# Kernel optimization log

Hardware: AMD Instinct MI355X
Metric: run time of the kernel (lower is better)

The kernel has to match this reference:

```python
import jax, jax.numpy as jnp
import numpy as np

N = 20000   # nodes per type per hop
E = 200000  # edges per relation per hop
H = 512     # node_feature_hid_len
FU = 512    # raw user feature len
FI = 256    # raw item feature len
NUM_RES = 2
NUM_DNN = 2


def setup_inputs() -> dict:
    key = jax.random.key(0)
    ks = iter(jax.random.split(key, 64))
    p = lambda shape: jax.random.normal(next(ks), shape, dtype=jnp.float32) * 0.05
    inp = {}
    # features per hop per type
    for h in range(3):
        inp[f'feat_user_h{h}'] = jax.random.normal(next(ks), (N, FU), dtype=jnp.float32)
        inp[f'feat_item_h{h}'] = jax.random.normal(next(ks), (N, FI), dtype=jnp.float32)
    del inp['feat_user_h2_']; 


def _unused():
    pass

# rebuild setup_inputs cleanly (above stub replaced)

def setup_inputs() -> dict:
    key = jax.random.key(0)
    ks = iter(jax.random.split(key, 64))
    p = lambda shape: jax.random.normal(next(ks), shape, dtype=jnp.float32) * 0.05
    inp = {}
    for h in range(3):
        inp[f'feat_user_h{h}'] = jax.random.normal(next(ks), (N, FU), dtype=jnp.float32)
        inp[f'feat_item_h{h}'] = jax.random.normal(next(ks), (N, FI), dtype=jnp.float32)
    for name in ('edges_UI_h0', 'edges_IU_h0', 'edges_UI_h1', 'edges_IU_h1'):
        inp[name] = jax.random.randint(next(ks), (2, E), 0, N, dtype=jnp.int32)
    # per-node-type input transforms
    inp['W_user'] = p((FU, H)); inp['b_user'] = jnp.zeros((H,), jnp.float32)
    inp['W_item'] = p((FI, H)); inp['b_item'] = jnp.zeros((H,), jnp.float32)
    # per-relation GATConv params, stacked over 2 relations [UI, IU]
    inp['gat_feat_W'] = p((2, H, H)); inp['gat_feat_b'] = jnp.zeros((2, H), jnp.float32)
    inp['gat_att_w'] = p((2, 2 * H)); inp['gat_att_b'] = jnp.zeros((2,), jnp.float32)
    inp['gat_bias'] = jnp.zeros((2, H), jnp.float32)
    # Res_DNN params
    inp['prep_W'] = p((H, H)); inp['prep_b'] = jnp.zeros((H,), jnp.float32)
    inp['dnn_W'] = p((NUM_RES, NUM_DNN, H, H)); inp['dnn_b'] = jnp.zeros((NUM_RES, NUM_DNN, H), jnp.float32)
    inp['dnn_ln_g'] = jnp.ones((NUM_RES, NUM_DNN, H), jnp.float32); inp['dnn_ln_b'] = jnp.zeros((NUM_RES, NUM_DNN, H), jnp.float32)
    inp['res_ln_g'] = jnp.ones((NUM_RES, H), jnp.float32); inp['res_ln_b'] = jnp.zeros((NUM_RES, H), jnp.float32)
    inp['cls_W'] = p((H, 1)); inp['cls_b'] = jnp.zeros((1,), jnp.float32)
    return inp


def _ln(x, g, b, eps=1e-5):
    mu = jnp.mean(x, axis=-1, keepdims=True)
    var = jnp.mean((x - mu) ** 2, axis=-1, keepdims=True)
    return (x - mu) * jax.lax.rsqrt(var + eps) * g + b


def _gat(head_h, tail_h, edges, fW, fb, aw, ab, bias):
    # GATConv: feat_linear on both sides, tanh edge attention, per-source-row
    # sparse softmax, scatter-weighted sum of transformed tail features.
    s = head_h @ fW + fb            # [Nh, H]
    t = tail_h @ fW + fb            # [Nt, H]
    src, tgt = edges[0], edges[1]
    # att(cat([s_e, t_e])) split into per-node scores (same math as concat @ aw)
    e = jnp.tanh((s @ aw[:H])[src] + (t @ aw[H:])[tgt] + ab)  # [E]
    nh = head_h.shape[0]
    m = jax.ops.segment_max(e, src, num_segments=nh)
    ex = jnp.exp(e - m[src])
    den = jax.ops.segment_sum(ex, src, num_segments=nh)
    alpha = ex / den[src]
    hp = jax.ops.segment_sum(alpha[:, None] * t[tgt], src, num_segments=nh)
    return hp + bias


def _forward(feat_user_h0, feat_item_h0, feat_user_h1, feat_item_h1,
             feat_user_h2, feat_item_h2,
             W_user, b_user, W_item, b_item,
             gat_feat_W, gat_feat_b, gat_att_w, gat_att_b, gat_bias,
             prep_W, prep_b, dnn_W, dnn_b, dnn_ln_g, dnn_ln_b,
             res_ln_g, res_ln_b, cls_W, cls_b,
             edges_UI_h0, edges_IU_h0, edges_UI_h1, edges_IU_h1):
    def gat(r, head, tail, edges):
        return _gat(head, tail, edges, gat_feat_W[r], gat_feat_b[r],
                    gat_att_w[r], gat_att_b[r], gat_bias[r])
    # hop 2 (deepest): transformed source features
    su = feat_user_h2 @ W_user + b_user
    si = feat_item_h2 @ W_item + b_item
    # hop 1
    hu = feat_user_h1 @ W_user + b_user
    hi = feat_item_h1 @ W_item + b_item
    su_new = (hu + gat(0, hu, si, edges_UI_h1)) * 0.5  # mean of [self, UI agg]
    si_new = (hi + gat(1, hi, su, edges_IU_h1)) * 0.5
    su, si = su_new, si_new
    # hop 0
    hu = feat_user_h0 @ W_user + b_user
    hi = feat_item_h0 @ W_item + b_item
    su_new = (hu + gat(0, hu, si, edges_UI_h0)) * 0.5
    su = su_new  # target node type = 'user' (first key)
    # Res_DNN head
    x = su @ prep_W + prep_b
    for r in range(NUM_RES):
        sc = x
        for d in range(NUM_DNN):
            x = _ln(jnp.tanh(x @ dnn_W[r, d] + dnn_b[r, d]), dnn_ln_g[r, d], dnn_ln_b[r, d])
        x = _ln(jnp.tanh(sc + x), res_ln_g[r], res_ln_b[r])
    return jax.nn.sigmoid(x @ cls_W + cls_b)  # [N, 1]


def reference(feat_user_h0, feat_item_h0, feat_user_h1, feat_item_h1,
              feat_user_h2, feat_item_h2,
              edges_UI_h0, edges_IU_h0, edges_UI_h1, edges_IU_h1,
              W_user, b_user, W_item, b_item,
              gat_feat_W, gat_feat_b, gat_att_w, gat_att_b, gat_bias,
              prep_W, prep_b, dnn_W, dnn_b, dnn_ln_g, dnn_ln_b,
              res_ln_g, res_ln_b, cls_W, cls_b):
    return _forward(feat_user_h0, feat_item_h0, feat_user_h1, feat_item_h1,
                    feat_user_h2, feat_item_h2,
                    W_user, b_user, W_item, b_item,
                    gat_feat_W, gat_feat_b, gat_att_w, gat_att_b, gat_bias,
                    prep_W, prep_b, dnn_W, dnn_b, dnn_ln_g, dnn_ln_b,
                    res_ln_g, res_ln_b, cls_W, cls_b,
                    edges_UI_h0, edges_IU_h0, edges_UI_h1, edges_IU_h1)
```

## Files before the change

kernel.cpp:

```cpp
#include <hip/hip_runtime.h>
#include <math.h>

#define NN 20000
#define NE 200000
#define HH 512

typedef __attribute__((ext_vector_type(8))) short short8v;
typedef __attribute__((ext_vector_type(4))) float f32x4;

__device__ inline short f2bf(float f) {
    union { float f; unsigned u; } v; v.f = f;
    unsigned r = (v.u + 0x7fffu + ((v.u >> 16) & 1u)) >> 16;
    return (short)r;
}
__device__ inline float bf2f(short s) {
    union { unsigned u; float f; } v;
    v.u = ((unsigned)(unsigned short)s) << 16;
    return v.f;
}

__device__ inline void gload_lds16(const void* g, void* l) {
    __builtin_amdgcn_global_load_lds(
        (const __attribute__((address_space(1))) void*)g,
        (__attribute__((address_space(3))) void*)l, 16, 0, 0);
}

__global__ __launch_bounds__(256)
void f2b_all(const float* __restrict__ fu2, const float* __restrict__ fu0,
             const float* __restrict__ fi1, short* __restrict__ S0,
             short* __restrict__ XI1, int nh8)
{
    int i = blockIdx.x * 256 + threadIdx.x;
    const float* src; short* dst; int off;
    if (i < nh8)            { src = fu2; dst = S0;                    off = i; }
    else if (i < 2 * nh8)   { src = fu0; dst = S0 + (size_t)nh8 * 8;  off = i - nh8; }
    else if (i < 2 * nh8 + nh8 / 2) { src = fi1; dst = XI1;           off = i - 2 * nh8; }
    else return;
    const float4* p = (const float4*)src + (size_t)off * 2;
    float4 a = p[0], b = p[1];
    short8v s;
    s[0] = f2bf(a.x); s[1] = f2bf(a.y); s[2] = f2bf(a.z); s[3] = f2bf(a.w);
    s[4] = f2bf(b.x); s[5] = f2bf(b.y); s[6] = f2bf(b.z); s[7] = f2bf(b.w);
    ((short8v*)dst)[off] = s;
}

__global__ __launch_bounds__(256)
void wtr_all(const float* __restrict__ Wu, const float* __restrict__ Wi,
             const float* __restrict__ gfW, const float* __restrict__ prW,
             const float* __restrict__ dW,
             short* __restrict__ WTu, short* __restrict__ WTi,
             short* __restrict__ WTg0, short* __restrict__ WTg1,
             short* __restrict__ WTpr, short* __restrict__ WTd)
{
    __shared__ float t[32][33];
    int z = blockIdx.z;
    const float* src; short* dst; int K;
    if (z == 0)      { src = Wu;  dst = WTu;  K = 512; }
    else if (z == 1) { src = Wi;  dst = WTi;  K = 256; }
    else if (z == 2) { src = gfW; dst = WTg0; K = 512; }
    else if (z == 3) { src = gfW + (size_t)512 * 512; dst = WTg1; K = 512; }
    else if (z == 4) { src = prW; dst = WTpr; K = 512; }
    else { src = dW + (size_t)(z - 5) * 512 * 512;
           dst = WTd + (size_t)(z - 5) * 512 * 512; K = 512; }
    int by = blockIdx.y * 32;
    if (by >= K) return;
    int bx = blockIdx.x * 32;
    int tx = threadIdx.x, ty = threadIdx.y;
    for (int i = ty; i < 32; i += 8)
        t[i][tx] = src[(size_t)(by + i) * 512 + bx + tx];
    __syncthreads();
    for (int i = ty; i < 32; i += 8)
        dst[(size_t)(bx + i) * K + by + tx] = f2bf(t[tx][i]);
}

__global__ __launch_bounds__(256)
void mfma_lin(const short* __restrict__ X, const short* __restrict__ WT,
              const float* __restrict__ bias, float* __restrict__ outF,
              short* __restrict__ outB, int M, int K,
              const short* __restrict__ rdH, const short* __restrict__ rdT,
              const float* __restrict__ rduv, const float* __restrict__ rds0,
              float* __restrict__ rdss, float* __restrict__ rdts, int rdN)
{
    __shared__ short8v pool[4096];

    const int tid = threadIdx.x;
    const int lane = tid & 63;
    const int w = tid >> 6;

    const int nby = (M + 127) >> 7;
    const int nwg = nby << 2;
    int id = blockIdx.x;

    if (id >= nwg) {
        int row = (id - nwg) * 4 + w;
        if (row >= rdN) return;
        short8v h = ((const short8v*)(rdH + (size_t)row * HH))[lane];
        short8v t = ((const short8v*)(rdT + (size_t)row * HH))[lane];
        const float4* up = (const float4*)rduv + lane * 2;
        const float4* vp = (const float4*)(rduv + HH) + lane * 2;
        float4 u0 = up[0], u1 = up[1], v0 = vp[0], v1 = vp[1];
        float a = bf2f(h[0])*u0.x + bf2f(h[1])*u0.y + bf2f(h[2])*u0.z + bf2f(h[3])*u0.w
                + bf2f(h[4])*u1.x + bf2f(h[5])*u1.y + bf2f(h[6])*u1.z + bf2f(h[7])*u1.w;
        float b = bf2f(t[0])*v0.x + bf2f(t[1])*v0.y + bf2f(t[2])*v0.z + bf2f(t[3])*v0.w
                + bf2f(t[4])*v1.x + bf2f(t[5])*v1.y + bf2f(t[6])*v1.z + bf2f(t[7])*v1.w;
#pragma unroll
        for (int m = 32; m >= 1; m >>= 1) {
            a += __shfl_xor(a, m);
            b += __shfl_xor(b, m);
        }
        if (lane == 0) { rdss[row] = a + rds0[0]; rdts[row] = b + rds0[1]; }
        return;
    }

    const int q = nwg >> 3, r = nwg & 7;
    int xcd = id & 7, wi = id >> 3;
    int wgid = (xcd < r ? xcd * (q + 1) : r * (q + 1) + (xcd - r) * q) + wi;
    const int col0 = (wgid & 3) * 128;
    const int row0 = (wgid >> 2) * 128;

    const int wr = (w >> 1) * 64;
    const int wc = (w & 1) * 64;

    const short* gsrc[8];
#pragma unroll
    for (int g = 0; g < 8; ++g) {
        int p = w * 512 + g * 64 + lane;
        if (p < 1024) {
            int row = p >> 3;
            int c = (p & 7) ^ (row & 7);
            int ga = row0 + row; if (ga >= M) ga = M - 1;
            gsrc[g] = X + (size_t)ga * K + c * 8;
        } else {
            int qq = p - 1024;
            int col = qq >> 3;
            int c = (qq & 7) ^ (col & 7);
            gsrc[g] = WT + (size_t)(col0 + col) * K + c * 8;
        }
    }

    int ar[2][4], br[2][4];
#pragma unroll
    for (int kk = 0; kk < 2; ++kk) {
#pragma unroll
        for (int i = 0; i < 4; ++i) {
            int rr = wr + i * 16 + (lane & 15);
            ar[kk][i] = rr * 8 + ((kk * 4 + (lane >> 4)) ^ (rr & 7));
            int nn = wc + i * 16 + (lane & 15);
            br[kk][i] = 1024 + nn * 8 + ((kk * 4 + (lane >> 4)) ^ (nn & 7));
        }
    }

    f32x4 acc[4][4];
#pragma unroll
    for (int i = 0; i < 4; ++i)
#pragma unroll
        for (int j = 0; j < 4; ++j)
            acc[i][j] = (f32x4){0.f, 0.f, 0.f, 0.f};

    auto stage = [&](int buf, int kk) {
        short8v* base = pool + buf * 2048 + w * 512;
#pragma unroll
        for (int g = 0; g < 8; ++g)
            gload_lds16(gsrc[g] + kk, base + g * 64);
    };

    const int nt = K >> 6;
    stage(0, 0);
    if (nt > 1) stage(1, 64);
    int cur = 0;
    for (int t = 0; t < nt; ++t) {
        if (t + 1 < nt) asm volatile("s_waitcnt vmcnt(8)" ::: "memory");
        else            asm volatile("s_waitcnt vmcnt(0)" ::: "memory");
        __builtin_amdgcn_s_barrier();
        const short8v* S = pool + cur * 2048;
#pragma unroll
        for (int kk = 0; kk < 2; ++kk) {
            short8v af[4], bf[4];
#pragma unroll
            for (int i = 0; i < 4; ++i) af[i] = S[ar[kk][i]];
#pragma unroll
            for (int j = 0; j < 4; ++j) bf[j] = S[br[kk][j]];
#pragma unroll
            for (int i = 0; i < 4; ++i)
#pragma unroll
                for (int j = 0; j < 4; ++j)
                    acc[i][j] = __builtin_amdgcn_mfma_f32_16x16x32_bf16(af[i], bf[j], acc[i][j], 0, 0, 0);
        }
        __builtin_amdgcn_s_barrier();
        if (t + 2 < nt) stage(cur, (t + 2) * 64);
        cur ^= 1;
    }

    float bj[4];
#pragma unroll
    for (int j = 0; j < 4; ++j)
        bj[j] = bias[col0 + wc + j * 16 + (lane & 15)];

    if (outF) {
#pragma unroll
        for (int i = 0; i < 4; ++i) {
#pragma unroll
            for (int rr = 0; rr < 4; ++rr) {
                int row = row0 + wr + i * 16 + (lane >> 4) * 4 + rr;
                if (row < M) {
                    float* op = outF + (size_t)row * HH + col0 + wc + (lane & 15);
#pragma unroll
                    for (int j = 0; j < 4; ++j) op[j * 16] = acc[i][j][rr] + bj[j];
                }
            }
        }
    }
    if (outB) {
        short* lt = (short*)pool;
#pragma unroll
        for (int i = 0; i < 4; ++i)
#pragma unroll
            for (int rr = 0; rr < 4; ++rr) {
                int lrow = wr + i * 16 + (lane >> 4) * 4 + rr;
#pragma unroll
                for (int j = 0; j < 4; ++j)
                    lt[lrow * 128 + wc + j * 16 + (lane & 15)] = f2bf(acc[i][j][rr] + bj[j]);
            }
        __syncthreads();
#pragma unroll
        for (int k = 0; k < 8; ++k) {
            int row = (tid >> 4) + 16 * k;
            int seg = tid & 15;
            int grow = row0 + row;
            if (grow < M) {
                short8v vv = *(short8v*)(lt + row * 128 + seg * 8);
                *(short8v*)(outB + (size_t)grow * HH + col0 + seg * 8) = vv;
            }
        }
    }
}

__global__ __launch_bounds__(256)
void gat_pre2(const float* __restrict__ gfW, const float* __restrict__ gfb,
              const float* __restrict__ gaw, float* __restrict__ uvall,
              float* __restrict__ s0t0all)
{
    int rrel = blockIdx.y;
    const float* fW = gfW + (size_t)rrel * HH * HH;
    const float* fb = gfb + rrel * HH;
    const float* aw = gaw + (size_t)rrel * 2 * HH;
    float* uv = uvall + rrel * 1024;
    float* s0t0 = s0t0all + rrel * 4;
    int row = blockIdx.x * 4 + (threadIdx.x >> 6);
    int lane = threadIdx.x & 63;
    const float4* ah = (const float4*)aw;
    const float4* at = (const float4*)(aw + HH);
    const float4* fp;
    if (row < 512)       fp = (const float4*)(fW + (size_t)row * HH);
    else if (row == 512) fp = (const float4*)fb;
    else return;
    float du = 0.f, dv = 0.f;
#pragma unroll
    for (int l = 0; l < 2; ++l) {
        int idx = lane * 2 + l;
        float4 f = fp[idx], a = ah[idx], b = at[idx];
        du += f.x*a.x + f.y*a.y + f.z*a.z + f.w*a.w;
        dv += f.x*b.x + f.y*b.y + f.z*b.z + f.w*b.w;
    }
#pragma unroll
    for (int m = 32; m >= 1; m >>= 1) {
        du += __shfl_xor(du, m);
        dv += __shfl_xor(dv, m);
    }
    if (lane == 0) {
        if (row < 512) { uv[row] = du; uv[512 + row] = dv; }
        else           { s0t0[0] = du; s0t0[1] = dv; }
    }
}

__global__ __launch_bounds__(256)
void count2_kernel(const int* __restrict__ s0, const int* __restrict__ s1,
                   int* __restrict__ c0, int* __restrict__ c1, int E)
{
    int i = blockIdx.x * blockDim.x + threadIdx.x;
    if (i < E) atomicAdd(&c0[s0[i]], 1);
    else if (i < 2 * E) atomicAdd(&c1[s1[i - E]], 1);
}

__global__ __launch_bounds__(1024)
void scan2_kernel(const int* __restrict__ c0, const int* __restrict__ c1,
                  int* __restrict__ o0, int* __restrict__ o1,
                  int* __restrict__ u0, int* __restrict__ u1, int n)
{
    const int* counts = blockIdx.x ? c1 : c0;
    int* offs = blockIdx.x ? o1 : o0;
    int* curs = blockIdx.x ? u1 : u0;
    __shared__ int part[1024];
    const int tid = threadIdx.x;
    const int CH = (n + 1023) / 1024;
    const int base = tid * CH;
    int s = 0;
    for (int i = 0; i < CH; ++i) {
        int idx = base + i;
        if (idx < n) s += counts[idx];
    }
    part[tid] = s;
    __syncthreads();
    for (int d = 1; d < 1024; d <<= 1) {
        int v = 0;
        if (tid >= d) v = part[tid - d];
        __syncthreads();
        if (tid >= d) part[tid] += v;
        __syncthreads();
    }
    int run = (tid == 0) ? 0 : part[tid - 1];
    for (int i = 0; i < CH; ++i) {
        int idx = base + i;
        if (idx < n) { offs[idx] = run; curs[idx] = run; run += counts[idx]; }
    }
    if (tid == 1023) offs[n] = run;
}

__global__ __launch_bounds__(256)
void fill_kernel(const int* __restrict__ src, const int* __restrict__ tgt,
                 const float* __restrict__ ss, const float* __restrict__ ts,
                 const float* __restrict__ ab_ptr, int* __restrict__ cursor,
                 int* __restrict__ tvals, float* __restrict__ wv,
                 int* __restrict__ eidx, int E)
{
    int i = blockIdx.x * blockDim.x + threadIdx.x;
    if (i >= E) return;
    int s = src[i], t = tgt[i];
    int pos = atomicAdd(&cursor[s], 1);
    tvals[pos] = t;
    wv[pos] = expf(tanhf(ss[s] + ts[t] + ab_ptr[0]));
    eidx[pos] = i;
}

__global__ __launch_bounds__(256)
void sortbkt_kernel(const int* __restrict__ offs, int* __restrict__ tvals,
                    float* __restrict__ wv, const int* __restrict__ eidx, int N)
{
    __shared__ int   lt[4][512];
    __shared__ float lw[4][512];
    int w = threadIdx.x >> 6, lane = threadIdx.x & 63;
    int s = blockIdx.x * 4 + w;
    if (s >= N) return;
    int beg = offs[s], end = offs[s + 1];
    int L = end - beg;
    if (L <= 1) return;
    if (L <= 64) {
        int e = 0x7fffffff, t = 0; float fw = 0.f;
        if (lane < L) { e = eidx[beg + lane]; t = tvals[beg + lane]; fw = wv[beg + lane]; }
        int r = 0;
        for (int k = 0; k < L; ++k) {
            int ek = __shfl(e, k);
            r += (ek < e) ? 1 : 0;
        }
        if (lane < L) { tvals[beg + r] = t; wv[beg + r] = fw; }
    } else if (L <= 512) {
        for (int j = lane; j < L; j += 64) { lt[w][j] = tvals[beg + j]; lw[w][j] = wv[beg + j]; }
        asm volatile("s_waitcnt lgkmcnt(0) vmcnt(0)" ::: "memory");
        for (int j = lane; j < L; j += 64) {
            int e = eidx[beg + j];
            int r = 0;
            for (int k = 0; k < L; ++k) r += (eidx[beg + k] < e) ? 1 : 0;
            tvals[beg + r] = lt[w][j]; wv[beg + r] = lw[w][j];
        }
    }
}

__global__ __launch_bounds__(256)
void gat_agg_kernel(const int* __restrict__ offs, const int* __restrict__ tvals,
                    const float* __restrict__ wv, const short* __restrict__ T,
                    const short* __restrict__ head, const float* __restrict__ gbias,
                    short* __restrict__ out, int N)
{
    int s = blockIdx.x * 4 + (threadIdx.x >> 6);
    int lane = threadIdx.x & 63;
    if (s >= N) return;
    const int beg = offs[s], end = offs[s + 1];
    float a[8];
#pragma unroll
    for (int q = 0; q < 8; ++q) a[q] = 0.f;
    float den = 0.f;

    int j = beg;
    for (; j + 4 <= end; j += 4) {
        int t0 = tvals[j], t1 = tvals[j + 1], t2 = tvals[j + 2], t3 = tvals[j + 3];
        float w0 = wv[j], w1 = wv[j + 1], w2 = wv[j + 2], w3 = wv[j + 3];
        short8v v0 = ((const short8v*)(T + (size_t)t0 * HH))[lane];
        short8v v1 = ((const short8v*)(T + (size_t)t1 * HH))[lane];
        short8v v2 = ((const short8v*)(T + (size_t)t2 * HH))[lane];
        short8v v3 = ((const short8v*)(T + (size_t)t3 * HH))[lane];
        den += w0 + w1 + w2 + w3;
#pragma unroll
        for (int q = 0; q < 8; ++q) {
            float acc = a[q];
            acc = fmaf(w0, bf2f(v0[q]), acc);
            acc = fmaf(w1, bf2f(v1[q]), acc);
            acc = fmaf(w2, bf2f(v2[q]), acc);
            acc = fmaf(w3, bf2f(v3[q]), acc);
            a[q] = acc;
        }
    }
    for (; j < end; ++j) {
        int t = tvals[j];
        float w = wv[j];
        short8v tv = ((const short8v*)(T + (size_t)t * HH))[lane];
        den += w;
#pragma unroll
        for (int q = 0; q < 8; ++q) a[q] = fmaf(w, bf2f(tv[q]), a[q]);
    }
    float inv = (den > 0.f) ? 1.f / den : 0.f;

    short8v h = ((const short8v*)(head + (size_t)s * HH))[lane];
    const float4* bp = (const float4*)gbias + lane * 2;
    float4 b0 = bp[0], b1 = bp[1];
    float bb[8] = {b0.x, b0.y, b0.z, b0.w, b1.x, b1.y, b1.z, b1.w};
    short8v o;
#pragma unroll
    for (int q = 0; q < 8; ++q)
        o[q] = f2bf((bf2f(h[q]) + a[q] * inv + bb[q]) * 0.5f);
    ((short8v*)(out + (size_t)s * HH))[lane] = o;
}

__global__ __launch_bounds__(256)
void tanh_ln_kernel(const short* __restrict__ Z,
                    const float* __restrict__ g, const float* __restrict__ bta,
                    short* __restrict__ outB, int N)
{
    int row = blockIdx.x * 4 + (threadIdx.x >> 6);
    int lane = threadIdx.x & 63;
    if (row >= N) return;
    short8v zv = ((const short8v*)(Z + (size_t)row * HH))[lane];
    float v[8];
    float sum = 0.f, sum2 = 0.f;
#pragma unroll
    for (int q = 0; q < 8; ++q) {
        float t = tanhf(bf2f(zv[q]));
        v[q] = t; sum += t; sum2 = fmaf(t, t, sum2);
    }
#pragma unroll
    for (int m = 32; m >= 1; m >>= 1) {
        sum += __shfl_xor(sum, m); sum2 += __shfl_xor(sum2, m);
    }
    float mu = sum * (1.f/HH);
    float rs = rsqrtf(sum2 * (1.f/HH) - mu*mu + 1e-5f);
    const float4* gp = (const float4*)g + lane * 2;
    const float4* bp = (const float4*)bta + lane * 2;
    float4 g0 = gp[0], g1 = gp[1], c0 = bp[0], c1 = bp[1];
    float gg[8] = {g0.x, g0.y, g0.z, g0.w, g1.x, g1.y, g1.z, g1.w};
    float cc[8] = {c0.x, c0.y, c0.z, c0.w, c1.x, c1.y, c1.z, c1.w};
    short8v ob;
#pragma unroll
    for (int q = 0; q < 8; ++q) ob[q] = f2bf((v[q]-mu)*rs*gg[q] + cc[q]);
    ((short8v*)(outB + (size_t)row * HH))[lane] = ob;
}

__global__ __launch_bounds__(256)
void tanh_ln2_kernel(const short* __restrict__ Z, const float* __restrict__ sc,
                     const float* __restrict__ g1, const float* __restrict__ b1,
                     const float* __restrict__ g2, const float* __restrict__ b2,
                     short* __restrict__ outB, float* __restrict__ outF,
                     const float* __restrict__ cWp, const float* __restrict__ cbp,
                     float* __restrict__ outCls, int N)
{
    int row = blockIdx.x * 4 + (threadIdx.x >> 6);
    int lane = threadIdx.x & 63;
    if (row >= N) return;
    short8v zv = ((const short8v*)(Z + (size_t)row * HH))[lane];
    float v[8];
    float sum = 0.f, sum2 = 0.f;
#pragma unroll
    for (int q = 0; q < 8; ++q) {
        float t = tanhf(bf2f(zv[q]));
        v[q] = t; sum += t; sum2 = fmaf(t, t, sum2);
    }
#pragma unroll
    for (int m = 32; m >= 1; m >>= 1) {
        sum += __shfl_xor(sum, m); sum2 += __shfl_xor(sum2, m);
    }
    float mu = sum * (1.f/HH);
    float rs = rsqrtf(sum2 * (1.f/HH) - mu*mu + 1e-5f);
    {
        const float4* gp = (const float4*)g1 + lane * 2;
        const float4* bp = (const float4*)b1 + lane * 2;
        float4 g0 = gp[0], g1v = gp[1], c0 = bp[0], c1 = bp[1];
        float gg[8] = {g0.x, g0.y, g0.z, g0.w, g1v.x, g1v.y, g1v.z, g1v.w};
        float cc[8] = {c0.x, c0.y, c0.z, c0.w, c1.x, c1.y, c1.z, c1.w};
        const float4* sp = (const float4*)(sc + (size_t)row * HH) + lane * 2;
        float4 s0 = sp[0], s1 = sp[1];
        float ssv[8] = {s0.x, s0.y, s0.z, s0.w, s1.x, s1.y, s1.z, s1.w};
        sum = 0.f; sum2 = 0.f;
#pragma unroll
        for (int q = 0; q < 8; ++q) {
            float x2 = (v[q]-mu)*rs*gg[q] + cc[q];
            float t = tanhf(ssv[q] + x2);
            v[q] = t; sum += t; sum2 = fmaf(t, t, sum2);
        }
    }
#pragma unroll
    for (int m = 32; m >= 1; m >>= 1) {
        sum += __shfl_xor(sum, m); sum2 += __shfl_xor(sum2, m);
    }
    mu = sum * (1.f/HH);
    rs = rsqrtf(sum2 * (1.f/HH) - mu*mu + 1e-5f);
    const float4* gp = (const float4*)g2 + lane * 2;
    const float4* bp = (const float4*)b2 + lane * 2;
    float4 g0 = gp[0], g1v = gp[1], c0 = bp[0], c1 = bp[1];
    float gg[8] = {g0.x, g0.y, g0.z, g0.w, g1v.x, g1v.y, g1v.z, g1v.w};
    float cc[8] = {c0.x, c0.y, c0.z, c0.w, c1.x, c1.y, c1.z, c1.w};
    float o[8];
#pragma unroll
    for (int q = 0; q < 8; ++q) o[q] = (v[q]-mu)*rs*gg[q] + cc[q];
    if (outB) {
        short8v ob;
#pragma unroll
        for (int q = 0; q < 8; ++q) ob[q] = f2bf(o[q]);
        ((short8v*)(outB + (size_t)row * HH))[lane] = ob;
    }
    if (outF) {
        float4* op = (float4*)(outF + (size_t)row * HH) + lane * 2;
        op[0] = make_float4(o[0], o[1], o[2], o[3]);
        op[1] = make_float4(o[4], o[5], o[6], o[7]);
    }
    if (cWp) {
        const float4* wp = (const float4*)cWp + lane * 2;
        float4 w0 = wp[0], w1 = wp[1];
        float acc = o[0]*w0.x + o[1]*w0.y + o[2]*w0.z + o[3]*w0.w
                  + o[4]*w1.x + o[5]*w1.y + o[6]*w1.z + o[7]*w1.w;
#pragma unroll
        for (int m = 32; m >= 1; m >>= 1) acc += __shfl_xor(acc, m);
        if (lane == 0) outCls[row] = 1.f / (1.f + expf(-(acc + cbp[0])));
    }
}

extern "C" void kernel_launch(void* const* d_in, const int* in_sizes, int n_in,
                              void* d_out, int out_size, void* d_ws, size_t ws_size,
                              hipStream_t stream)
{
    (void)in_sizes; (void)n_in; (void)out_size; (void)ws_size;
    const int N = NN, E = NE, H = HH;
    const size_t NHf = (size_t)N * H;

    const float* fu0 = (const float*)d_in[0];
    const float* fi1 = (const float*)d_in[3];
    const float* fu2 = (const float*)d_in[4];
    const int* eUI0 = (const int*)d_in[6];
    const int* eIU1 = (const int*)d_in[9];
    const float* Wu  = (const float*)d_in[10];
    const float* bu  = (const float*)d_in[11];
    const float* Wi  = (const float*)d_in[12];
    const float* bi  = (const float*)d_in[13];
    const float* gfW = (const float*)d_in[14];
    const float* gfb = (const float*)d_in[15];
    const float* gaw = (const float*)d_in[16];
    const float* gab = (const float*)d_in[17];
    const float* gbias = (const float*)d_in[18];
    const float* prW = (const float*)d_in[19];
    const float* prb = (const float*)d_in[20];
    const float* dW  = (const float*)d_in[21];
    const float* db  = (const float*)d_in[22];
    const float* dlg = (const float*)d_in[23];
    const float* dlb = (const float*)d_in[24];
    const float* rlg = (const float*)d_in[25];
    const float* rlb = (const float*)d_in[26];
    const float* cW  = (const float*)d_in[27];
    const float* cb  = (const float*)d_in[28];

    float* B5     = (float*)d_ws;
    float* ssb    = B5 + NHf;
    float* tsb    = ssb + N;
    float* uvall  = tsb + N;
    float* s0t0a  = uvall + 2048;
    float* wvb    = s0t0a + 8;
    int* counts0 = (int*)(wvb + E);
    int* counts1 = counts0 + N;
    int* offs0   = counts1 + N;
    int* offs1   = offs0 + N + 1;
    int* cur0    = offs1 + N + 1;
    int* cur1    = cur0 + N;
    int* tvals   = cur1 + N;
    int* eidxb   = tvals + E;
    size_t boff = (size_t)((char*)(eidxb + E) - (char*)d_ws);
    boff = (boff + 15) & ~(size_t)15;
    short* S0    = (short*)((char*)d_ws + boff);
    short* SUHU  = S0 + 2 * NHf;
    short* XI1   = SUHU + 2 * NHf;
    short* HI    = XI1 + NHf / 2;
    short* SINEW = HI + NHf;
    short* T4    = SINEW + NHf;
    short* SUF   = T4 + NHf;
    short* WTu   = SUF + NHf;
    short* WTi   = WTu + 512 * 512;
    short* WTg0  = WTi + 512 * 256;
    short* WTg1  = WTg0 + 512 * 512;
    short* WTpr  = WTg1 + 512 * 512;
    short* WTd   = WTpr + 512 * 512;
    short* SU  = SUHU;
    short* HU0 = SUHU + NHf;
    short* XB  = SINEW;
    short* ZB  = SU;

    hipLaunchKernelGGL(wtr_all, dim3(16, 16, 9), dim3(32, 8), 0, stream,
                       Wu, Wi, gfW, prW, dW, WTu, WTi, WTg0, WTg1, WTpr, WTd);
    int nh8 = (int)(NHf / 8);
    int ftot = 2 * nh8 + nh8 / 2;
    hipLaunchKernelGGL(f2b_all, dim3((ftot + 255) / 256), dim3(256), 0, stream,
                       fu2, fu0, fi1, S0, XI1, nh8);
    hipMemsetAsync(counts0, 0, 2 * N * sizeof(int), stream);
    hipLaunchKernelGGL(count2_kernel, dim3((2 * E + 255) / 256), dim3(256), 0, stream,
                       eUI0, eIU1, counts0, counts1, E);
    hipLaunchKernelGGL(scan2_kernel, dim3(2), dim3(1024), 0, stream,
                       counts0, counts1, offs0, offs1, cur0, cur1, N);
    hipLaunchKernelGGL(gat_pre2, dim3(130, 2), dim3(256), 0, stream,
                       gfW, gfb, gaw, uvall, s0t0a);

    const int rgrid = (N + 3) / 4;
    const int egrid = (E + 255) / 256;
    auto MLIN = [&](const short* X, const short* WT, const float* b,
                    float* oF, short* oB, int M, int K,
                    const short* rdH, const short* rdT, const float* rduv,
                    const float* rds0) {
        int nwg = ((M + 127) / 128) * 4;
        int grid = nwg + (rdH ? rgrid : 0);
        hipLaunchKernelGGL(mfma_lin, dim3(grid), dim3(256), 0, stream,
                           X, WT, b, oF, oB, M, K,
                           rdH, rdT, rduv, rds0, ssb, tsb, N);
    };

    auto GAT = [&](int r, const short* headB, const short* tailB, const short* WTg,
                   const int* edges, int* offs, int* curs, short* outB) {
        MLIN(tailB, WTg, gfb + r * H, nullptr, T4, N, 512,
             headB, tailB, uvall + r * 1024, s0t0a + r * 4);
        hipLaunchKernelGGL(fill_kernel, dim3(egrid), dim3(256), 0, stream,
                           edges, edges + E, ssb, tsb, gab + r, curs, tvals, wvb,
                           eidxb, E);
        hipLaunchKernelGGL(sortbkt_kernel, dim3(rgrid), dim3(256), 0, stream,
                           offs, tvals, wvb, eidxb, N);
        hipLaunchKernelGGL(gat_agg_kernel, dim3(rgrid), dim3(256), 0, stream,
                           offs, tvals, wvb, T4, headB, gbias + (size_t)r * H, outB, N);
    };

    MLIN(S0, WTu, bu, nullptr, SUHU, 2 * N, 512, nullptr, nullptr, nullptr, nullptr);
    MLIN(XI1, WTi, bi, nullptr, HI, N, 256, nullptr, nullptr, nullptr, nullptr);
    GAT(1, HI, SU, WTg1, eIU1, offs1, cur1, SINEW);
    GAT(0, HU0, SINEW, WTg0, eUI0, offs0, cur0, SUF);

    MLIN(SUF, WTpr, prb, B5, XB, N, 512, nullptr, nullptr, nullptr, nullptr);
    for (int r = 0; r < 2; ++r) {
        MLIN(XB, WTd + (size_t)(r * 2) * 512 * 512, db + (r * 2) * H,
             nullptr, ZB, N, 512, nullptr, nullptr, nullptr, nullptr);
        hipLaunchKernelGGL(tanh_ln_kernel, dim3(rgrid), dim3(256), 0, stream,
                           ZB, dlg + (r * 2) * H, dlb + (r * 2) * H, XB, N);
        MLIN(XB, WTd + (size_t)(r * 2 + 1) * 512 * 512, db + (r * 2 + 1) * H,
             nullptr, ZB, N, 512, nullptr, nullptr, nullptr, nullptr);
        if (r == 0) {
            hipLaunchKernelGGL(tanh_ln2_kernel, dim3(rgrid), dim3(256), 0, stream,
                               ZB, B5, dlg + H, dlb + H, rlg, rlb,
                               XB, B5, (const float*)nullptr, (const float*)nullptr,
                               (float*)nullptr, N);
        } else {
            hipLaunchKernelGGL(tanh_ln2_kernel, dim3(rgrid), dim3(256), 0, stream,
                               ZB, B5, dlg + 3 * H, dlb + 3 * H, rlg + H, rlb + H,
                               (short*)nullptr, (float*)nullptr, cW, cb,
                               (float*)d_out, N);
        }
    }
}
```

Baseline: 516.1 us.

## Fuse fp32-to-bf16 feature conversion into input-projection GEMM loads

Removes the separate f2b_all conversion kernel and adds mfma_linf, which streams fp32 features straight into LDS with a swizzle and converts them to bf16 in registers just before the MFMAs. This drops one full read-and-write pass over the bf16 staging buffers and one kernel launch. In exchange the GEMM reads fp32 A tiles (twice the bytes per tile) and does the conversion inside the inner loop. The LDS row stride of the epilogue transpose also changes from 128 to 136 to reduce bank conflicts.

```diff
diff --git a/kernel.cpp b/kernel.cpp
--- a/kernel.cpp
+++ b/kernel.cpp
@@ -23,25 +23,6 @@
     __builtin_amdgcn_global_load_lds(
         (const __attribute__((address_space(1))) void*)g,
         (__attribute__((address_space(3))) void*)l, 16, 0, 0);
-}
-
-__global__ __launch_bounds__(256)
-void f2b_all(const float* __restrict__ fu2, const float* __restrict__ fu0,
-             const float* __restrict__ fi1, short* __restrict__ S0,
-             short* __restrict__ XI1, int nh8)
-{
-    int i = blockIdx.x * 256 + threadIdx.x;
-    const float* src; short* dst; int off;
-    if (i < nh8)            { src = fu2; dst = S0;                    off = i; }
-    else if (i < 2 * nh8)   { src = fu0; dst = S0 + (size_t)nh8 * 8;  off = i - nh8; }
-    else if (i < 2 * nh8 + nh8 / 2) { src = fi1; dst = XI1;           off = i - 2 * nh8; }
-    else return;
-    const float4* p = (const float4*)src + (size_t)off * 2;
-    float4 a = p[0], b = p[1];
-    short8v s;
-    s[0] = f2bf(a.x); s[1] = f2bf(a.y); s[2] = f2bf(a.z); s[3] = f2bf(a.w);
-    s[4] = f2bf(b.x); s[5] = f2bf(b.y); s[6] = f2bf(b.z); s[7] = f2bf(b.w);
-    ((short8v*)dst)[off] = s;
 }
 
 __global__ __launch_bounds__(256)
@@ -219,7 +200,7 @@
                 int lrow = wr + i * 16 + (lane >> 4) * 4 + rr;
 #pragma unroll
                 for (int j = 0; j < 4; ++j)
-                    lt[lrow * 128 + wc + j * 16 + (lane & 15)] = f2bf(acc[i][j][rr] + bj[j]);
+                    lt[lrow * 136 + wc + j * 16 + (lane & 15)] = f2bf(acc[i][j][rr] + bj[j]);
             }
         __syncthreads();
 #pragma unroll
@@ -228,9 +209,143 @@
             int seg = tid & 15;
             int grow = row0 + row;
             if (grow < M) {
-                short8v vv = *(short8v*)(lt + row * 128 + seg * 8);
+                short8v vv = *(short8v*)(lt + row * 136 + seg * 8);
                 *(short8v*)(outB + (size_t)grow * HH + col0 + seg * 8) = vv;
             }
+        }
+    }
+}
+
+__global__ __launch_bounds__(256)
+void mfma_linf(const float* __restrict__ XA, const float* __restrict__ XB2,
+               int NA, const short* __restrict__ WT,
+               const float* __restrict__ bias, short* __restrict__ outB,
+               int M, int K)
+{
+    __shared__ short8v pool[3072];
+
+    const int tid = threadIdx.x;
+    const int lane = tid & 63;
+    const int w = tid >> 6;
+
+    const int nby = (M + 127) >> 7;
+    const int nwg = nby << 2;
+    const int q = nwg >> 3, r = nwg & 7;
+    int id = blockIdx.x;
+    int xcd = id & 7, wi = id >> 3;
+    int wgid = (xcd < r ? xcd * (q + 1) : r * (q + 1) + (xcd - r) * q) + wi;
+    const int col0 = (wgid & 3) * 128;
+    const int row0 = (wgid >> 2) * 128;
+
+    const int wr = (w >> 1) * 64;
+    const int wc = (w & 1) * 64;
+    const int kg = lane >> 4;
+
+    const float* ga_[4];
+#pragma unroll
+    for (int g = 0; g < 4; ++g) {
+        int p = w * 256 + g * 64 + lane;
+        int row = p >> 3;
+        int c = (p & 7) ^ (row & 7);
+        int ga = row0 + row; if (ga >= M) ga = M - 1;
+        const float* base = (ga < NA) ? XA + (size_t)ga * K
+                                      : XB2 + (size_t)(ga - NA) * K;
+        ga_[g] = base + c * 4;
+    }
+    const short* gb_[2];
+#pragma unroll
+    for (int g = 0; g < 2; ++g) {
+        int p = w * 128 + g * 64 + lane;
+        int col = p >> 2;
+        int c = (p & 3) ^ ((col >> 1) & 3);
+        gb_[g] = WT + (size_t)(col0 + col) * K + c * 8;
+    }
+
+    int arow[4], br_[4];
+#pragma unroll
+    for (int i = 0; i < 4; ++i) arow[i] = wr + i * 16 + (lane & 15);
+#pragma unroll
+    for (int j = 0; j < 4; ++j) {
+        int nn = wc + j * 16 + (lane & 15);
+        br_[j] = 1024 + nn * 4 + (kg ^ ((nn >> 1) & 3));
+    }
+
+    f32x4 acc[4][4];
+#pragma unroll
+    for (int i = 0; i < 4; ++i)
+#pragma unroll
+        for (int j = 0; j < 4; ++j)
+            acc[i][j] = (f32x4){0.f, 0.f, 0.f, 0.f};
+
+    auto stage = [&](int buf, int t) {
+        short8v* base = pool + buf * 1536 + w * 256;
+#pragma unroll
+        for (int g = 0; g < 4; ++g)
+            gload_lds16(ga_[g] + t * 32, base + g * 64);
+        short8v* bb = pool + buf * 1536 + 1024 + w * 128;
+#pragma unroll
+        for (int g = 0; g < 2; ++g)
+            gload_lds16(gb_[g] + t * 32, bb + g * 64);
+    };
+
+    const int nt = K >> 5;
+    stage(0, 0);
+    if (nt > 1) stage(1, 1);
+    int cur = 0;
+    for (int t = 0; t < nt; ++t) {
+        if (t + 1 < nt) asm volatile("s_waitcnt vmcnt(6)" ::: "memory");
+        else            asm volatile("s_waitcnt vmcnt(0)" ::: "memory");
+        __builtin_amdgcn_s_barrier();
+        const float4* Af = (const float4*)(pool + cur * 1536);
+        const short8v* S = pool + cur * 1536;
+        short8v af[4], bf[4];
+#pragma unroll
+        for (int i = 0; i < 4; ++i) {
+            int rr = arow[i];
+            int s = rr & 7;
+            float4 lo = Af[rr * 8 + ((2 * kg)     ^ s)];
+            float4 hi = Af[rr * 8 + ((2 * kg + 1) ^ s)];
+            af[i][0] = f2bf(lo.x); af[i][1] = f2bf(lo.y);
+            af[i][2] = f2bf(lo.z); af[i][3] = f2bf(lo.w);
+            af[i][4] = f2bf(hi.x); af[i][5] = f2bf(hi.y);
+            af[i][6] = f2bf(hi.z); af[i][7] = f2bf(hi.w);
+        }
+#pragma unroll
+        for (int j = 0; j < 4; ++j) bf[j] = S[br_[j]];
+#pragma unroll
+        for (int i = 0; i < 4; ++i)
+#pragma unroll
+            for (int j = 0; j < 4; ++j)
+                acc[i][j] = __builtin_amdgcn_mfma_f32_16x16x32_bf16(af[i], bf[j], acc[i][j], 0, 0, 0);
+        __builtin_amdgcn_s_barrier();
+        if (t + 2 < nt) stage(cur, t + 2);
+        cur ^= 1;
+    }
+
+    float bj[4];
+#pragma unroll
+    for (int j = 0; j < 4; ++j)
+        bj[j] = bias[col0 + wc + j * 16 + (lane & 15)];
+
+    short* lt = (short*)pool;
+#pragma unroll
+    for (int i = 0; i < 4; ++i)
+#pragma unroll
+        for (int rr = 0; rr < 4; ++rr) {
+            int lrow = wr + i * 16 + (lane >> 4) * 4 + rr;
+#pragma unroll
+            for (int j = 0; j < 4; ++j)
+                lt[lrow * 136 + wc + j * 16 + (lane & 15)] = f2bf(acc[i][j][rr] + bj[j]);
+        }
+    __syncthreads();
+#pragma unroll
+    for (int k = 0; k < 8; ++k) {
+        int row = (tid >> 4) + 16 * k;
+        int seg = tid & 15;
+        int grow = row0 + row;
+        if (grow < M) {
+            short8v vv = *(short8v*)(lt + row * 136 + seg * 8);
+            *(short8v*)(outB + (size_t)grow * HH + col0 + seg * 8) = vv;
         }
     }
 }
@@ -580,10 +695,8 @@
     int* eidxb   = tvals + E;
     size_t boff = (size_t)((char*)(eidxb + E) - (char*)d_ws);
     boff = (boff + 15) & ~(size_t)15;
-    short* S0    = (short*)((char*)d_ws + boff);
-    short* SUHU  = S0 + 2 * NHf;
-    short* XI1   = SUHU + 2 * NHf;
-    short* HI    = XI1 + NHf / 2;
+    short* SUHU  = (short*)((char*)d_ws + boff);
+    short* HI    = SUHU + 2 * NHf;
     short* SINEW = HI + NHf;
     short* T4    = SINEW + NHf;
     short* SUF   = T4 + NHf;
@@ -600,10 +713,6 @@
 
     hipLaunchKernelGGL(wtr_all, dim3(16, 16, 9), dim3(32, 8), 0, stream,
                        Wu, Wi, gfW, prW, dW, WTu, WTi, WTg0, WTg1, WTpr, WTd);
-    int nh8 = (int)(NHf / 8);
-    int ftot = 2 * nh8 + nh8 / 2;
-    hipLaunchKernelGGL(f2b_all, dim3((ftot + 255) / 256), dim3(256), 0, stream,
-                       fu2, fu0, fi1, S0, XI1, nh8);
     hipMemsetAsync(counts0, 0, 2 * N * sizeof(int), stream);
     hipLaunchKernelGGL(count2_kernel, dim3((2 * E + 255) / 256), dim3(256), 0, stream,
                        eUI0, eIU1, counts0, counts1, E);
@@ -624,6 +733,12 @@
                            X, WT, b, oF, oB, M, K,
                            rdH, rdT, rduv, rds0, ssb, tsb, N);
     };
+    auto MLINF = [&](const float* XA, const float* XB2, int NA, const short* WT,
+                     const float* b, short* oB, int M, int K) {
+        int nwg = ((M + 127) / 128) * 4;
+        hipLaunchKernelGGL(mfma_linf, dim3(nwg), dim3(256), 0, stream,
+                           XA, XB2, NA, WT, b, oB, M, K);
+    };
 
     auto GAT = [&](int r, const short* headB, const short* tailB, const short* WTg,
                    const int* edges, int* offs, int* curs, short* outB) {
@@ -638,8 +753,8 @@
                            offs, tvals, wvb, T4, headB, gbias + (size_t)r * H, outB, N);
     };
 
-    MLIN(S0, WTu, bu, nullptr, SUHU, 2 * N, 512, nullptr, nullptr, nullptr, nullptr);
-    MLIN(XI1, WTi, bi, nullptr, HI, N, 256, nullptr, nullptr, nullptr, nullptr);
+    MLINF(fu2, fu0, N, WTu, bu, SUHU, 2 * N, 512);
+    MLINF(fi1, fi1, N, WTi, bi, HI, N, 256);
     GAT(1, HI, SU, WTg1, eIU1, offs1, cur1, SINEW);
     GAT(0, HU0, SINEW, WTg0, eUI0, offs0, cur0, SUF);
 
```

Result: no change. 512.5 us (-0.7%).
